# Optimization experiments

Measured on AMD Instinct MI355X. Metric: run time of the kernel, lower is better.

## Reference

```python
import jax, jax.numpy as jnp
import numpy as np

B, S, E, H = 4, 1024, 1024, 16
D = E // H  # head_dim


def setup_inputs() -> dict:
    key = jax.random.key(0)
    ks = jax.random.split(key, 12)
    s = 1.0 / np.sqrt(E)
    return {
        "value": jax.random.normal(ks[0], (B, S, E), jnp.float32),
        "key_in": jax.random.normal(ks[1], (B, S, E), jnp.float32),
        "query": jax.random.normal(ks[2], (B, S, E), jnp.float32),
        "mask": jax.random.randint(ks[3], (B, 1, 1, S), 0, 2, jnp.int32),
        "Wq": jax.random.normal(ks[4], (E, E), jnp.float32) * s,
        "bq": jnp.zeros((E,), jnp.float32),
        "Wk": jax.random.normal(ks[5], (E, E), jnp.float32) * s,
        "bk": jnp.zeros((E,), jnp.float32),
        "Wv": jax.random.normal(ks[6], (E, E), jnp.float32) * s,
        "bv": jnp.zeros((E,), jnp.float32),
        "Wo": jax.random.normal(ks[7], (E, E), jnp.float32) * s,
        "bo": jnp.zeros((E,), jnp.float32),
    }


def reference(value, key_in, query, mask, Wq, bq, Wk, bk, Wv, bv, Wo, bo):
    b = query.shape[0]
    # torch Linear: y = x @ W.T + b
    Q = (query @ Wq.T + bq).reshape(b, query.shape[1], H, D)
    K = (key_in @ Wk.T + bk).reshape(b, key_in.shape[1], H, D)
    V = (value @ Wv.T + bv).reshape(b, value.shape[1], H, D)
    # scores scaled by 1/sqrt(embed_dim) (faithful to source, not head_dim)
    energy = jnp.einsum("bqhd,bkhd->bhqk", Q, K) / jnp.sqrt(jnp.float32(E))
    energy = jnp.where(mask == 0, jnp.float32(-1e20), energy)
    attention = jax.nn.softmax(energy, axis=-1)
    out = jnp.einsum("bhqk,bkhd->bqhd", attention, V).reshape(b, query.shape[1], E)
    return out @ Wo.T + bo
```

## Files before the change

### kernel.cpp

```cpp
#include <hip/hip_runtime.h>


typedef unsigned short u16;
typedef __bf16 bf16x8 __attribute__((ext_vector_type(8)));
typedef short s16x4 __attribute__((ext_vector_type(4)));
typedef float f32x4 __attribute__((ext_vector_type(4)));

struct alignas(8) us4_t { u16 x, y, z, w; };

__device__ __forceinline__ u16 f2bf(float x) {
  unsigned int u = __builtin_bit_cast(unsigned int, x);
  unsigned int r = u + 0x7fffu + ((u >> 16) & 1u);
  return (u16)(r >> 16);
}

__device__ __forceinline__ f32x4 zero4() {
  f32x4 z; z[0] = 0.f; z[1] = 0.f; z[2] = 0.f; z[3] = 0.f; return z;
}

__device__ __forceinline__ void async_copy16(const void* g, void* l) {
  __builtin_amdgcn_global_load_lds(
      (__attribute__((address_space(1))) void*)(uintptr_t)g,
      (__attribute__((address_space(3))) void*)l, 16, 0, 0);
}

__global__ void fused_cast(const float* __restrict__ q, const float* __restrict__ k,
                           const float* __restrict__ v, const float* __restrict__ wq,
                           const float* __restrict__ wk, const float* __restrict__ wv,
                           const float* __restrict__ wo, const int* __restrict__ mask,
                           u16* __restrict__ qo, u16* __restrict__ ko, u16* __restrict__ vo,
                           u16* __restrict__ wqo, u16* __restrict__ wko, u16* __restrict__ wvo,
                           u16* __restrict__ woo, float* __restrict__ biasf) {
  const int blk = blockIdx.x;
  if (blk >= 16384) {
    int i = (blk - 16384) * 256 + threadIdx.x;
    biasf[i] = mask[i] ? 0.f : -1.4427e20f;
    return;
  }
  const float* src; u16* dst; int off;
  if (blk < 4096)       { src = q;  dst = qo;  off = blk; }
  else if (blk < 8192)  { src = k;  dst = ko;  off = blk - 4096; }
  else if (blk < 12288) { src = v;  dst = vo;  off = blk - 8192; }
  else if (blk < 13312) { src = wq; dst = wqo; off = blk - 12288; }
  else if (blk < 14336) { src = wk; dst = wko; off = blk - 13312; }
  else if (blk < 15360) { src = wv; dst = wvo; off = blk - 14336; }
  else                  { src = wo; dst = woo; off = blk - 15360; }
  const size_t i = (size_t)off * 256 + threadIdx.x;
  float4 f = ((const float4*)src)[i];
  us4_t o;
  o.x = f2bf(f.x); o.y = f2bf(f.y); o.z = f2bf(f.z); o.w = f2bf(f.w);
  ((us4_t*)dst)[i] = o;
}

template <bool OUT_BF16>
__device__ __forceinline__ void gemm_core(const u16* __restrict__ A,
                                          const u16* __restrict__ Bw,
                                          const float* __restrict__ bias,
                                          void* __restrict__ outp, bool trans) {
  __shared__ u16 lA[128 * 64];
  __shared__ u16 lB[128 * 64];
  const int tid = threadIdx.x;
  const int lane = tid & 63, w = tid >> 6;
  const int wm = w >> 1, wn = w & 1;
  const int quad = lane >> 4, l16 = lane & 15;
  const int rg = lane >> 3, cs = lane & 7;
  const int m0 = blockIdx.y * 128, n0 = blockIdx.x * 128;

  f32x4 acc[4][4];
#pragma unroll
  for (int i = 0; i < 4; ++i)
#pragma unroll
    for (int j = 0; j < 4; ++j) acc[i][j] = zero4();

  for (int it = 0; it < 16; ++it) {
    const int k0 = it * 64;
#pragma unroll
    for (int t = 0; t < 4; ++t) {
      const int row = w * 32 + t * 8 + rg;
      const int c = cs ^ (row & 7);
      async_copy16(A + (size_t)(m0 + row) * 1024 + k0 + c * 8, &lA[(w * 32 + t * 8) * 64]);
      async_copy16(Bw + (size_t)(n0 + row) * 1024 + k0 + c * 8, &lB[(w * 32 + t * 8) * 64]);
    }
    __syncthreads();
#pragma unroll
    for (int kk = 0; kk < 2; ++kk) {
      bf16x8 af[4], bfr[4];
#pragma unroll
      for (int i = 0; i < 4; ++i) {
        const int row = wm * 64 + i * 16 + l16;
        af[i] = *(const bf16x8*)&lA[row * 64 + (((kk * 4 + quad) ^ (row & 7)) * 8)];
      }
#pragma unroll
      for (int j = 0; j < 4; ++j) {
        const int row = wn * 64 + j * 16 + l16;
        bfr[j] = *(const bf16x8*)&lB[row * 64 + (((kk * 4 + quad) ^ (row & 7)) * 8)];
      }
#pragma unroll
      for (int i = 0; i < 4; ++i)
#pragma unroll
        for (int j = 0; j < 4; ++j)
          acc[i][j] = __builtin_amdgcn_mfma_f32_16x16x32_bf16(af[i], bfr[j], acc[i][j], 0, 0, 0);
    }
    __syncthreads();
  }

#pragma unroll
  for (int j = 0; j < 4; ++j) {
    const int cg = n0 + wn * 64 + j * 16 + l16;
    const float bj = bias[cg];
#pragma unroll
    for (int i = 0; i < 4; ++i) {
      const f32x4 v = acc[i][j];
      const int r0 = m0 + wm * 64 + i * 16 + quad * 4;
      if (!trans) {
        if (OUT_BF16) {
          u16* o = (u16*)outp;
#pragma unroll
          for (int r = 0; r < 4; ++r) o[(size_t)(r0 + r) * 1024 + cg] = f2bf(v[r] + bj);
        } else {
          float* o = (float*)outp;
#pragma unroll
          for (int r = 0; r < 4; ++r) o[(size_t)(r0 + r) * 1024 + cg] = v[r] + bj;
        }
      } else {
        u16* o = (u16*)outp;
        us4_t pk;
        pk.x = f2bf(v[0] + bj); pk.y = f2bf(v[1] + bj);
        pk.z = f2bf(v[2] + bj); pk.w = f2bf(v[3] + bj);
        *(us4_t*)&o[(size_t)(r0 >> 10) * 1048576 + (size_t)cg * 1024 + (r0 & 1023)] = pk;
      }
    }
  }
}

__global__ __launch_bounds__(256, 2) void qkv_gemm(
    const u16* __restrict__ Xq, const u16* __restrict__ Xk, const u16* __restrict__ Xv,
    const u16* __restrict__ Wq, const u16* __restrict__ Wk, const u16* __restrict__ Wv,
    const float* __restrict__ bq, const float* __restrict__ bk, const float* __restrict__ bv,
    u16* __restrict__ Qo, u16* __restrict__ Ko, u16* __restrict__ Vto) {
  const int z = blockIdx.z;
  const u16* A = (z == 0) ? Xq : (z == 1) ? Xk : Xv;
  const u16* W = (z == 0) ? Wq : (z == 1) ? Wk : Wv;
  const float* bias = (z == 0) ? bq : (z == 1) ? bk : bv;
  u16* out = (z == 0) ? Qo : (z == 1) ? Ko : Vto;
  gemm_core<true>(A, W, bias, out, z == 2);
}

__global__ __launch_bounds__(256, 2) void out_gemm(
    const u16* __restrict__ A, const u16* __restrict__ W,
    const float* __restrict__ bias, float* __restrict__ out) {
  gemm_core<false>(A, W, bias, out, false);
}

__global__ __launch_bounds__(256, 4) void attn_kernel(
    const u16* __restrict__ Qb, const u16* __restrict__ Kb, const u16* __restrict__ Vtb,
    const float* __restrict__ biasf, u16* __restrict__ Ob) {
  __shared__ u16 lK[128 * 64];
  __shared__ u16 lV[64 * 128];
  __shared__ u16 lQ[64 * 64];

  const int tid = threadIdx.x;
  const int lane = tid & 63, w = tid >> 6;
  const int quad = lane >> 4, l16 = lane & 15;
  const int rg = lane >> 3, cs = lane & 7;
  const int bh = blockIdx.x, qt = blockIdx.y;
  const int b = bh >> 4;
  const size_t qkBase = (size_t)b * 1048576 + (size_t)(bh & 15) * 64;
  const float C = 0.0450842200277982f;

#pragma unroll
  for (int t = 0; t < 2; ++t) {
    const int row = w * 16 + t * 8 + rg;
    const int c = cs ^ (row & 7);
    async_copy16(Qb + qkBase + (size_t)(qt * 64 + row) * 1024 + c * 8,
                 &lQ[(w * 16 + t * 8) * 64]);
  }
  __syncthreads();

  bf16x8 qf[2];
#pragma unroll
  for (int kk = 0; kk < 2; ++kk) {
    const int row = w * 16 + l16;
    qf[kk] = *(const bf16x8*)&lQ[row * 64 + (((kk * 4 + quad) ^ (row & 7)) * 8)];
  }

  float m2 = -3.0e38f, lsum = 0.f;
  f32x4 oacc[4];
#pragma unroll
  for (int dt = 0; dt < 4; ++dt) oacc[dt] = zero4();

  for (int it = 0; it < 8; ++it) {
    const int k0 = it * 128;
#pragma unroll
    for (int t = 0; t < 4; ++t) {
      const int row = w * 32 + t * 8 + rg;
      const int c = cs ^ (row & 7);
      async_copy16(Kb + qkBase + (size_t)(k0 + row) * 1024 + c * 8,
                   &lK[(w * 32 + t * 8) * 64]);
    }
#pragma unroll
    for (int t = 0; t < 4; ++t) {
      const int d0 = w * 16 + t * 4 + quad;
      const int c = l16 ^ (d0 & 15);
      async_copy16(Vtb + (size_t)(bh * 64 + d0) * 1024 + k0 + c * 8,
                   &lV[(w * 16 + t * 4) * 128]);
    }
    __syncthreads();

    f32x4 sacc[8];
#pragma unroll
    for (int n = 0; n < 8; ++n) sacc[n] = zero4();
#pragma unroll
    for (int kk = 0; kk < 2; ++kk) {
#pragma unroll
      for (int n = 0; n < 8; ++n) {
        const int row = n * 16 + l16;
        bf16x8 kf = *(const bf16x8*)&lK[row * 64 + (((kk * 4 + quad) ^ (row & 7)) * 8)];
        sacc[n] = __builtin_amdgcn_mfma_f32_16x16x32_bf16(kf, qf[kk], sacc[n], 0, 0, 0);
      }
    }

#pragma unroll
    for (int n = 0; n < 8; ++n) {
      const float4 vb = *(const float4*)&biasf[b * 1024 + k0 + n * 16 + quad * 4];
      sacc[n][0] = fmaf(sacc[n][0], C, vb.x);
      sacc[n][1] = fmaf(sacc[n][1], C, vb.y);
      sacc[n][2] = fmaf(sacc[n][2], C, vb.z);
      sacc[n][3] = fmaf(sacc[n][3], C, vb.w);
    }

    f32x4 m4 = sacc[0];
#pragma unroll
    for (int n = 1; n < 8; ++n) {
      m4[0] = fmaxf(m4[0], sacc[n][0]); m4[1] = fmaxf(m4[1], sacc[n][1]);
      m4[2] = fmaxf(m4[2], sacc[n][2]); m4[3] = fmaxf(m4[3], sacc[n][3]);
    }
    float rm = fmaxf(fmaxf(m4[0], m4[1]), fmaxf(m4[2], m4[3]));
    rm = fmaxf(rm, __shfl_xor(rm, 16));
    rm = fmaxf(rm, __shfl_xor(rm, 32));
    const float mn = fmaxf(m2, rm);
    const float alpha = __builtin_amdgcn_exp2f(m2 - mn);
    m2 = mn;

    f32x4 sum4 = zero4();
#pragma unroll
    for (int n = 0; n < 8; ++n) {
#pragma unroll
      for (int r = 0; r < 4; ++r) {
        const float p = __builtin_amdgcn_exp2f(sacc[n][r] - mn);
        sacc[n][r] = p;
        sum4[r] += p;
      }
    }
    float rs = (sum4[0] + sum4[1]) + (sum4[2] + sum4[3]);
    rs += __shfl_xor(rs, 16);
    rs += __shfl_xor(rs, 32);
    lsum = lsum * alpha + rs;
#pragma unroll
    for (int dt = 0; dt < 4; ++dt) {
      oacc[dt][0] *= alpha; oacc[dt][1] *= alpha;
      oacc[dt][2] *= alpha; oacc[dt][3] *= alpha;
    }

    s16x4 pf[8];
#pragma unroll
    for (int n = 0; n < 8; ++n) {
      pf[n][0] = (short)f2bf(sacc[n][0]);
      pf[n][1] = (short)f2bf(sacc[n][1]);
      pf[n][2] = (short)f2bf(sacc[n][2]);
      pf[n][3] = (short)f2bf(sacc[n][3]);
    }

#pragma unroll
    for (int dt = 0; dt < 4; ++dt) {
      const int row = dt * 16 + l16;
#pragma unroll
      for (int ks = 0; ks < 8; ++ks) {
        const int chunk = ks * 2 + (quad >> 1);
        s16x4 vf = *(const s16x4*)&lV[row * 128 + ((chunk ^ (row & 15)) * 8) + (quad & 1) * 4];
        oacc[dt] = __builtin_amdgcn_mfma_f32_16x16x16bf16_1k(vf, pf[ks], oacc[dt], 0, 0, 0);
      }
    }
    __syncthreads();
  }

  const float inv = 1.f / lsum;
  const int qg = qt * 64 + w * 16 + l16;
#pragma unroll
  for (int dt = 0; dt < 4; ++dt) {
    us4_t pk;
    pk.x = f2bf(oacc[dt][0] * inv);
    pk.y = f2bf(oacc[dt][1] * inv);
    pk.z = f2bf(oacc[dt][2] * inv);
    pk.w = f2bf(oacc[dt][3] * inv);
    *(us4_t*)&Ob[qkBase + (size_t)qg * 1024 + dt * 16 + quad * 4] = pk;
  }
}

extern "C" void kernel_launch(void* const* d_in, const int* in_sizes, int n_in,
                              void* d_out, int out_size, void* d_ws, size_t ws_size,
                              hipStream_t stream) {
  const float* value  = (const float*)d_in[0];
  const float* key_in = (const float*)d_in[1];
  const float* query  = (const float*)d_in[2];
  const int*   mask   = (const int*)d_in[3];
  const float* Wq = (const float*)d_in[4];
  const float* bq = (const float*)d_in[5];
  const float* Wk = (const float*)d_in[6];
  const float* bk = (const float*)d_in[7];
  const float* Wv = (const float*)d_in[8];
  const float* bv = (const float*)d_in[9];
  const float* Wo = (const float*)d_in[10];
  const float* bo = (const float*)d_in[11];

  u16* ws = (u16*)d_ws;
  u16* q_bf  = ws;
  u16* k_bf  = ws + 4194304;
  u16* v_bf  = ws + 8388608;
  u16* wq_bf = ws + 12582912;
  u16* wk_bf = ws + 13631488;
  u16* wv_bf = ws + 14680064;
  u16* wo_bf = ws + 15728640;
  u16* Qbuf  = ws + 16777216;
  u16* Kbuf  = ws + 20971520;
  u16* Vtbuf = ws + 25165824;
  u16* attnb = ws + 29360128;
  float* biasf = (float*)d_out;

  fused_cast<<<16400, 256, 0, stream>>>(query, key_in, value, Wq, Wk, Wv, Wo, mask,
                                        q_bf, k_bf, v_bf, wq_bf, wk_bf, wv_bf, wo_bf,
                                        biasf);
  qkv_gemm<<<dim3(8, 32, 3), 256, 0, stream>>>(q_bf, k_bf, v_bf, wq_bf, wk_bf, wv_bf,
                                               bq, bk, bv, Qbuf, Kbuf, Vtbuf);
  attn_kernel<<<dim3(64, 16), 256, 0, stream>>>(Qbuf, Kbuf, Vtbuf, biasf, attnb);
  out_gemm<<<dim3(8, 32, 1), 256, 0, stream>>>(attnb, wo_bf, bo, (float*)d_out);
}
```

Before: 219.6 us.

## Pre-swizzle V layout, alias Q in LDS, remap blocks per XCD, packed bf16 cvt

The QKV GEMM now writes V in a layout grouped by four keys, so the attention kernel can load each V tile as a contiguous linear copy and read MFMA operands without XOR swizzle. Q staging reuses the V shared buffer, which needs an extra barrier but lowers LDS use per block. Attention blocks are remapped onto a flat grid so that each XCD handles contiguous batch-head groups, aiming to improve L2 reuse of K and V. Manual bf16 rounding is replaced by a packed hardware conversion builtin when it is available. The new unswizzled V reads may cause LDS bank conflicts.

```diff
diff --git a/kernel.cpp b/kernel.cpp
--- a/kernel.cpp
+++ b/kernel.cpp
@@ -3,6 +3,7 @@
 
 typedef unsigned short u16;
 typedef __bf16 bf16x8 __attribute__((ext_vector_type(8)));
+typedef __bf16 bf16x2 __attribute__((ext_vector_type(2)));
 typedef short s16x4 __attribute__((ext_vector_type(4)));
 typedef float f32x4 __attribute__((ext_vector_type(4)));
 
@@ -12,6 +13,15 @@
   unsigned int u = __builtin_bit_cast(unsigned int, x);
   unsigned int r = u + 0x7fffu + ((u >> 16) & 1u);
   return (u16)(r >> 16);
+}
+
+__device__ __forceinline__ unsigned int pack2bf(float a, float b) {
+#if __has_builtin(__builtin_amdgcn_cvt_pk_bf16_f32)
+  bf16x2 r = __builtin_amdgcn_cvt_pk_bf16_f32(a, b);
+  return __builtin_bit_cast(unsigned int, r);
+#else
+  return (unsigned int)f2bf(a) | ((unsigned int)f2bf(b) << 16);
+#endif
 }
 
 __device__ __forceinline__ f32x4 zero4() {
@@ -47,9 +57,9 @@
   else                  { src = wo; dst = woo; off = blk - 15360; }
   const size_t i = (size_t)off * 256 + threadIdx.x;
   float4 f = ((const float4*)src)[i];
-  us4_t o;
-  o.x = f2bf(f.x); o.y = f2bf(f.y); o.z = f2bf(f.z); o.w = f2bf(f.w);
-  ((us4_t*)dst)[i] = o;
+  unsigned int lo = pack2bf(f.x, f.y), hi = pack2bf(f.z, f.w);
+  unsigned long long pk = (unsigned long long)lo | ((unsigned long long)hi << 32);
+  ((unsigned long long*)dst)[i] = pk;
 }
 
 template <bool OUT_BF16>
@@ -124,10 +134,13 @@
         }
       } else {
         u16* o = (u16*)outp;
-        us4_t pk;
-        pk.x = f2bf(v[0] + bj); pk.y = f2bf(v[1] + bj);
-        pk.z = f2bf(v[2] + bj); pk.w = f2bf(v[3] + bj);
-        *(us4_t*)&o[(size_t)(r0 >> 10) * 1048576 + (size_t)cg * 1024 + (r0 & 1023)] = pk;
+        const int bh = ((r0 >> 10) << 4) + (cg >> 6);
+        const int g  = (r0 & 1023) >> 2;
+        const int d  = cg & 63;
+        union { us4_t s; unsigned int u[2]; } pk;
+        pk.u[0] = pack2bf(v[0] + bj, v[1] + bj);
+        pk.u[1] = pack2bf(v[2] + bj, v[3] + bj);
+        *(us4_t*)&o[(size_t)bh * 65536 + g * 256 + d * 4] = pk.s;
       }
     }
   }
@@ -157,15 +170,19 @@
     const float* __restrict__ biasf, u16* __restrict__ Ob) {
   __shared__ u16 lK[128 * 64];
   __shared__ u16 lV[64 * 128];
-  __shared__ u16 lQ[64 * 64];
+  u16* lQ = lV;
 
   const int tid = threadIdx.x;
   const int lane = tid & 63, w = tid >> 6;
   const int quad = lane >> 4, l16 = lane & 15;
   const int rg = lane >> 3, cs = lane & 7;
-  const int bh = blockIdx.x, qt = blockIdx.y;
+
+  const int flat = blockIdx.x;
+  const int xcd = flat & 7, r = flat >> 3;
+  const int bh = xcd * 8 + (r & 7), qt = r >> 3;
   const int b = bh >> 4;
   const size_t qkBase = (size_t)b * 1048576 + (size_t)(bh & 15) * 64;
+  const size_t vBase = (size_t)bh * 65536;
   const float C = 0.0450842200277982f;
 
 #pragma unroll
@@ -183,6 +200,7 @@
     const int row = w * 16 + l16;
     qf[kk] = *(const bf16x8*)&lQ[row * 64 + (((kk * 4 + quad) ^ (row & 7)) * 8)];
   }
+  __syncthreads();
 
   float m2 = -3.0e38f, lsum = 0.f;
   f32x4 oacc[4];
@@ -200,10 +218,8 @@
     }
 #pragma unroll
     for (int t = 0; t < 4; ++t) {
-      const int d0 = w * 16 + t * 4 + quad;
-      const int c = l16 ^ (d0 & 15);
-      async_copy16(Vtb + (size_t)(bh * 64 + d0) * 1024 + k0 + c * 8,
-                   &lV[(w * 16 + t * 4) * 128]);
+      const int o16 = (w * 4 + t) * 512 + lane * 8;
+      async_copy16(Vtb + vBase + (size_t)it * 8192 + o16, &lV[(w * 4 + t) * 512]);
     }
     __syncthreads();
 
@@ -246,10 +262,10 @@
 #pragma unroll
     for (int n = 0; n < 8; ++n) {
 #pragma unroll
-      for (int r = 0; r < 4; ++r) {
-        const float p = __builtin_amdgcn_exp2f(sacc[n][r] - mn);
-        sacc[n][r] = p;
-        sum4[r] += p;
+      for (int r2 = 0; r2 < 4; ++r2) {
+        const float p = __builtin_amdgcn_exp2f(sacc[n][r2] - mn);
+        sacc[n][r2] = p;
+        sum4[r2] += p;
       }
     }
     float rs = (sum4[0] + sum4[1]) + (sum4[2] + sum4[3]);
@@ -265,19 +281,18 @@
     s16x4 pf[8];
 #pragma unroll
     for (int n = 0; n < 8; ++n) {
-      pf[n][0] = (short)f2bf(sacc[n][0]);
-      pf[n][1] = (short)f2bf(sacc[n][1]);
-      pf[n][2] = (short)f2bf(sacc[n][2]);
-      pf[n][3] = (short)f2bf(sacc[n][3]);
+      union { s16x4 v; unsigned int u[2]; } pu;
+      pu.u[0] = pack2bf(sacc[n][0], sacc[n][1]);
+      pu.u[1] = pack2bf(sacc[n][2], sacc[n][3]);
+      pf[n] = pu.v;
     }
 
 #pragma unroll
     for (int dt = 0; dt < 4; ++dt) {
-      const int row = dt * 16 + l16;
+      const int dbase = (dt * 16 + l16) * 4;
 #pragma unroll
       for (int ks = 0; ks < 8; ++ks) {
-        const int chunk = ks * 2 + (quad >> 1);
-        s16x4 vf = *(const s16x4*)&lV[row * 128 + ((chunk ^ (row & 15)) * 8) + (quad & 1) * 4];
+        s16x4 vf = *(const s16x4*)&lV[(ks * 4 + quad) * 256 + dbase];
         oacc[dt] = __builtin_amdgcn_mfma_f32_16x16x16bf16_1k(vf, pf[ks], oacc[dt], 0, 0, 0);
       }
     }
@@ -288,12 +303,10 @@
   const int qg = qt * 64 + w * 16 + l16;
 #pragma unroll
   for (int dt = 0; dt < 4; ++dt) {
-    us4_t pk;
-    pk.x = f2bf(oacc[dt][0] * inv);
-    pk.y = f2bf(oacc[dt][1] * inv);
-    pk.z = f2bf(oacc[dt][2] * inv);
-    pk.w = f2bf(oacc[dt][3] * inv);
-    *(us4_t*)&Ob[qkBase + (size_t)qg * 1024 + dt * 16 + quad * 4] = pk;
+    union { us4_t s; unsigned int u[2]; } pk;
+    pk.u[0] = pack2bf(oacc[dt][0] * inv, oacc[dt][1] * inv);
+    pk.u[1] = pack2bf(oacc[dt][2] * inv, oacc[dt][3] * inv);
+    *(us4_t*)&Ob[qkBase + (size_t)qg * 1024 + dt * 16 + quad * 4] = pk.s;
   }
 }
 
@@ -332,6 +345,6 @@
                                         biasf);
   qkv_gemm<<<dim3(8, 32, 3), 256, 0, stream>>>(q_bf, k_bf, v_bf, wq_bf, wk_bf, wv_bf,
                                                bq, bk, bv, Qbuf, Kbuf, Vtbuf);
-  attn_kernel<<<dim3(64, 16), 256, 0, stream>>>(Qbuf, Kbuf, Vtbuf, biasf, attnb);
+  attn_kernel<<<dim3(1024), 256, 0, stream>>>(Qbuf, Kbuf, Vtbuf, biasf, attnb);
   out_gemm<<<dim3(8, 32, 1), 256, 0, stream>>>(attnb, wo_bf, bo, (float*)d_out);
 }
```

Result: faster. 213.1 us (-3.0%).
